# Optimization experiments

Measured on AMD Instinct MI355X. Metric: run time of the kernel, lower is better.

Reference implementation:

```python
import jax, jax.numpy as jnp
import numpy as np


def setup_inputs() -> dict:
    key = jax.random.key(0)
    k1, k2 = jax.random.split(key)
    B, D, L = 32, 64, 4096
    N_CB, K = 4, 512
    x_in = jax.random.normal(k1, (B, D, L), dtype=jnp.float32)
    # torch.rand(num_tokens, token_dim) per codebook -> uniform [0,1)
    codebooks = jax.random.uniform(k2, (N_CB, K, D), dtype=jnp.float32)
    return {"x_in": x_in, "codebooks": codebooks}


def _vq_select(x_res, emb):
    """Nearest-code quantization for one codebook.

    x_res: [B, D, L], emb: [K, D]
    Returns z_q [B, D, L], idx [B, L].
    """
    x_t = jnp.transpose(x_res, (0, 2, 1))  # [B, L, D]
    # squared euclidean distances via GEMM (same argmin as torch.cdist)
    d2 = (
        jnp.sum(x_t * x_t, axis=-1, keepdims=True)
        - 2.0 * jnp.einsum("bld,kd->blk", x_t, emb)
        + jnp.sum(emb * emb, axis=-1)
    )  # [B, L, K]
    idx = jnp.argmin(d2, axis=-1)  # [B, L]
    z_q = jnp.transpose(emb[idx], (0, 2, 1))  # [B, D, L]
    return z_q, idx


def reference(x_in, codebooks):
    """Residual VQ: per codebook quantize the residual, accumulate sums.

    Returns z_q_aggregated [B, n_cb, D, L] (cumulative sums) and
    indices [B, L, n_cb].
    """
    n_cb = codebooks.shape[0]
    x_res = x_in
    z_q = jnp.zeros_like(x_in)
    agg = []
    idx_list = []
    for c in range(n_cb):  # small fixed loop over codebooks
        z_q_ind, idx = _vq_select(x_res, codebooks[c])
        x_res = x_res - z_q_ind
        z_q = z_q + z_q_ind
        agg.append(z_q)
        idx_list.append(idx)
    z_q_aggregated = jnp.stack(agg, axis=1)  # [B, n_cb, D, L]
    indices = jnp.stack(idx_list, axis=-1)  # [B, L, n_cb]
    return z_q_aggregated, indices
```

## Files before the change

kernel.cpp:

```cpp
#include <hip/hip_runtime.h>


#define LL   4096
#define DD   64
#define KK   512
#define NCB  4
#define TB   32
#define NTHR 256
#define XS   36
#define ES   260
#define EBUFN (16 * ES)

#define ZQ_ELEMS (32LL * NCB * DD * LL)

__device__ __forceinline__ float np_pairwise_sq64(const float* p) {
#pragma clang fp contract(off)
    float r[8];
#pragma unroll
    for (int j = 0; j < 8; ++j) { float s = p[j] * p[j]; r[j] = s; }
#pragma unroll
    for (int i = 8; i < 64; i += 8)
#pragma unroll
        for (int j = 0; j < 8; ++j) { float s = p[i + j] * p[i + j]; r[j] = r[j] + s; }
    return ((r[0] + r[1]) + (r[2] + r[3])) + ((r[4] + r[5]) + (r[6] + r[7]));
}

__global__ void se_kernel(const float* __restrict__ cb, float* __restrict__ se) {
    int t = blockIdx.x * blockDim.x + threadIdx.x;
    if (t >= NCB * KK) return;
    se[t] = np_pairwise_sq64(cb + (size_t)t * DD);
}

__global__ __launch_bounds__(NTHR) void rvq_kernel(const float* __restrict__ x_in,
                                                   const float* __restrict__ cb,
                                                   const float* __restrict__ se,
                                                   float* __restrict__ out) {
    __shared__ float ebuf[EBUFN];
    __shared__ float x_lds[DD * XS];

    const int tid  = threadIdx.x;
    const int lane = tid & 63;
    const int w8   = (tid >> 6) << 3;

    const long T0 = (long)blockIdx.x * TB;
    const int b  = (int)(T0 >> 12);
    const int l0 = (int)(T0 & 4095);

    {
        const float* xb = x_in + (size_t)b * DD * LL + l0;
        const int dd0 = tid >> 3;
        const int t4  = (tid & 7) << 2;
#pragma unroll
        for (int it = 0; it < 2; ++it) {
            const int d = it * 32 + dd0;
            const float4 v = *reinterpret_cast<const float4*>(xb + (size_t)d * LL + t4);
            *reinterpret_cast<float4*>(&x_lds[d * XS + t4]) = v;
        }
    }

    const int sq = tid & 3;
    const int sk = tid >> 2;

    float4 sv0, sv1, sv2, sv3;
    {
        const float* ec = cb + (size_t)(sq << 2);
        sv0 = *reinterpret_cast<const float4*>(ec + (size_t)(sk +   0) * DD);
        sv1 = *reinterpret_cast<const float4*>(ec + (size_t)(sk +  64) * DD);
        sv2 = *reinterpret_cast<const float4*>(ec + (size_t)(sk + 128) * DD);
        sv3 = *reinterpret_cast<const float4*>(ec + (size_t)(sk + 192) * DD);
    }

    __syncthreads();

    float zq[8];
#pragma unroll
    for (int t = 0; t < 8; ++t) zq[t] = 0.f;

    const int sxj = lane & 7;
    const int sxt = lane >> 3;
    const int myt = lane & 7;
    const int da  = lane >> 3;

#pragma unroll 1
    for (int c = 0; c < NCB; ++c) {
        float a3;
        {
            float r;
            {
#pragma clang fp contract(off)
                float p = x_lds[sxj * XS + w8 + sxt];
                r = p * p;
#pragma unroll
                for (int i = 1; i < 8; ++i) {
                    float q = x_lds[(i * 8 + sxj) * XS + w8 + sxt];
                    r = r + q * q;
                }
            }
            float o1 = __shfl_xor(r, 1, 64);
            float a1 = r + o1;
            float o2 = __shfl_xor(a1, 2, 64);
            float a2 = a1 + o2;
            float o4 = __shfl_xor(a2, 4, 64);
            a3 = a2 + o4;
        }

        float b1v[8]; int b1i[8];
#pragma unroll
        for (int t = 0; t < 8; ++t) { b1v[t] = __builtin_inff(); b1i[t] = 0; }

        float acc[8][4];

#pragma unroll 1
        for (int s = 0; s < 8; ++s) {
            ebuf[(sq * 4 + 0) * ES + sk      ] = sv0.x;
            ebuf[(sq * 4 + 1) * ES + sk      ] = sv0.y;
            ebuf[(sq * 4 + 2) * ES + sk      ] = sv0.z;
            ebuf[(sq * 4 + 3) * ES + sk      ] = sv0.w;
            ebuf[(sq * 4 + 0) * ES + sk +  64] = sv1.x;
            ebuf[(sq * 4 + 1) * ES + sk +  64] = sv1.y;
            ebuf[(sq * 4 + 2) * ES + sk +  64] = sv1.z;
            ebuf[(sq * 4 + 3) * ES + sk +  64] = sv1.w;
            ebuf[(sq * 4 + 0) * ES + sk + 128] = sv2.x;
            ebuf[(sq * 4 + 1) * ES + sk + 128] = sv2.y;
            ebuf[(sq * 4 + 2) * ES + sk + 128] = sv2.z;
            ebuf[(sq * 4 + 3) * ES + sk + 128] = sv2.w;
            ebuf[(sq * 4 + 0) * ES + sk + 192] = sv3.x;
            ebuf[(sq * 4 + 1) * ES + sk + 192] = sv3.y;
            ebuf[(sq * 4 + 2) * ES + sk + 192] = sv3.z;
            ebuf[(sq * 4 + 3) * ES + sk + 192] = sv3.w;

            __syncthreads();

            {
                int nc = c, ns = s + 1;
                if (ns == 8) { nc = c + 1; ns = 0; }
                if (nc < NCB) {
                    const float* ec = cb + ((size_t)(nc * KK + (ns >> 2) * 256)) * DD
                                         + (size_t)((ns & 3) * 16 + (sq << 2));
                    sv0 = *reinterpret_cast<const float4*>(ec + (size_t)(sk +   0) * DD);
                    sv1 = *reinterpret_cast<const float4*>(ec + (size_t)(sk +  64) * DD);
                    sv2 = *reinterpret_cast<const float4*>(ec + (size_t)(sk + 128) * DD);
                    sv3 = *reinterpret_cast<const float4*>(ec + (size_t)(sk + 192) * DD);
                }
            }

            if ((s & 3) == 0) {
#pragma unroll
                for (int t = 0; t < 8; ++t)
#pragma unroll
                    for (int g = 0; g < 4; ++g) acc[t][g] = 0.f;
            }

            const int mbase = (s & 3) * 16;
#pragma unroll
            for (int dd = 0; dd < 16; ++dd) {
                const int d = mbase + dd;
                const float4 e4  = *reinterpret_cast<const float4*>(&ebuf[dd * ES + (lane << 2)]);
                const float4 xa  = *reinterpret_cast<const float4*>(&x_lds[d * XS + w8]);
                const float4 xb4 = *reinterpret_cast<const float4*>(&x_lds[d * XS + w8 + 4]);
#define FMA4(T, XV)                                   \
                acc[T][0] = fmaf(XV, e4.x, acc[T][0]); \
                acc[T][1] = fmaf(XV, e4.y, acc[T][1]); \
                acc[T][2] = fmaf(XV, e4.z, acc[T][2]); \
                acc[T][3] = fmaf(XV, e4.w, acc[T][3]);
                FMA4(0, xa.x)  FMA4(1, xa.y)  FMA4(2, xa.z)  FMA4(3, xa.w)
                FMA4(4, xb4.x) FMA4(5, xb4.y) FMA4(6, xb4.z) FMA4(7, xb4.w)
#undef FMA4
            }

            if ((s & 3) == 3) {
#pragma clang fp contract(off)
                const int kb = (s >> 2) * 256 + (lane << 2);
                const float4 se4 = *reinterpret_cast<const float4*>(&se[c * KK + kb]);
                const float sev[4] = {se4.x, se4.y, se4.z, se4.w};
#pragma unroll
                for (int t = 0; t < 8; ++t) {
                    const float sxv = __shfl(a3, t << 3, 64);
#pragma unroll
                    for (int g = 0; g < 4; ++g) {
                        const float twod = 2.0f * acc[t][g];
                        const float d2 = (sxv - twod) + sev[g];
                        if (d2 < b1v[t]) { b1v[t] = d2; b1i[t] = kb + g; }
                    }
                }
            }

            __syncthreads();
        }

#pragma unroll
        for (int t = 0; t < 8; ++t) {
            float v = b1v[t]; int i = b1i[t];
#pragma unroll
            for (int off = 32; off > 0; off >>= 1) {
                const float ov = __shfl_xor(v, off, 64);
                const int   oi = __shfl_xor(i, off, 64);
                if (ov < v || (ov == v && oi < i)) { v = ov; i = oi; }
            }
            b1i[t] = i;
        }

        int kown = 0;
#pragma unroll
        for (int t = 0; t < 8; ++t) if (myt == t) kown = b1i[t];

        {
#pragma clang fp contract(off)
            const float* erow = cb + ((size_t)(c * KK) + kown) * DD + da;
#pragma unroll
            for (int i = 0; i < 8; ++i) {
                const float ev = erow[i * 8];
                const int xi = (i * 8 + da) * XS + w8 + myt;
                x_lds[xi] = x_lds[xi] - ev;
                zq[i] = zq[i] + ev;
            }
        }

#pragma unroll
        for (int t = 0; t < 8; ++t)
            if (lane == t)
                out[ZQ_ELEMS + ((size_t)b * LL + l0 + w8 + t) * NCB + c] = (float)b1i[t];

#pragma unroll
        for (int i = 0; i < 8; ++i)
            ebuf[(i * 8 + da) * XS + w8 + myt] = zq[i];
        __syncthreads();
        {
            float* zo = out + (((size_t)b * NCB + c) * DD) * LL + l0;
            const int c4 = (tid & 7) << 2;
            const int d0 = tid >> 3;
#pragma unroll
            for (int p = 0; p < 2; ++p) {
                const int d = p * 32 + d0;
                const float4 v = *reinterpret_cast<const float4*>(&ebuf[d * XS + c4]);
                *reinterpret_cast<float4*>(zo + (size_t)d * LL + c4) = v;
            }
        }
        __syncthreads();
    }
}

extern "C" void kernel_launch(void* const* d_in, const int* in_sizes, int n_in,
                              void* d_out, int out_size, void* d_ws, size_t ws_size,
                              hipStream_t stream) {
    const float* x_in = (const float*)d_in[0];
    const float* cb   = (const float*)d_in[1];
    float* out = (float*)d_out;
    float* se  = (float*)d_ws;

    se_kernel<<<dim3((NCB * KK + 255) / 256), dim3(256), 0, stream>>>(cb, se);
    rvq_kernel<<<dim3((32 * LL) / TB), dim3(NTHR), 0, stream>>>(x_in, cb, se, out);
}
```

Baseline: 639.0 us.

## Double block tile to 64 tokens with 512 threads sharing each codebook slice

Each block now handles 64 tokens with 512 threads instead of 32 with 256, so each codebook slice staged in shared memory is reused by twice as many tokens and global codebook traffic per token halves. Staging loads per thread shrink to two float4s. The z_q output transpose is done in two halves through the smaller shared buffer, which adds barriers. The first accumulation step multiplies instead of zeroing then adding. Larger blocks give fewer resident blocks per CU and half as many blocks overall.

```diff
diff --git a/kernel.cpp b/kernel.cpp
--- a/kernel.cpp
+++ b/kernel.cpp
@@ -5,9 +5,9 @@
 #define DD   64
 #define KK   512
 #define NCB  4
-#define TB   32
-#define NTHR 256
-#define XS   36
+#define TB   64
+#define NTHR 512
+#define XS   68
 #define ES   260
 #define EBUFN (16 * ES)
 
@@ -35,7 +35,7 @@
                                                    const float* __restrict__ cb,
                                                    const float* __restrict__ se,
                                                    float* __restrict__ out) {
-    __shared__ float ebuf[EBUFN];
+    __shared__ float sbuf[EBUFN];
     __shared__ float x_lds[DD * XS];
 
     const int tid  = threadIdx.x;
@@ -48,27 +48,24 @@
 
     {
         const float* xb = x_in + (size_t)b * DD * LL + l0;
-        const int dd0 = tid >> 3;
-        const int t4  = (tid & 7) << 2;
 #pragma unroll
         for (int it = 0; it < 2; ++it) {
-            const int d = it * 32 + dd0;
-            const float4 v = *reinterpret_cast<const float4*>(xb + (size_t)d * LL + t4);
-            *reinterpret_cast<float4*>(&x_lds[d * XS + t4]) = v;
+            const int q = tid + it * NTHR;
+            const int d = q >> 4;
+            const int col = (q & 15) << 2;
+            const float4 v = *reinterpret_cast<const float4*>(xb + (size_t)d * LL + col);
+            *reinterpret_cast<float4*>(&x_lds[d * XS + col]) = v;
         }
     }
 
     const int sq = tid & 3;
     const int sk = tid >> 2;
-
-    float4 sv0, sv1, sv2, sv3;
-    {
-        const float* ec = cb + (size_t)(sq << 2);
-        sv0 = *reinterpret_cast<const float4*>(ec + (size_t)(sk +   0) * DD);
-        sv1 = *reinterpret_cast<const float4*>(ec + (size_t)(sk +  64) * DD);
-        sv2 = *reinterpret_cast<const float4*>(ec + (size_t)(sk + 128) * DD);
-        sv3 = *reinterpret_cast<const float4*>(ec + (size_t)(sk + 192) * DD);
-    }
+    const size_t toff = (size_t)sk * DD + (sq << 2);
+    const int r0 = (sq << 2) * ES + sk;
+
+    float4 sv0, sv1;
+    sv0 = *reinterpret_cast<const float4*>(cb + toff);
+    sv1 = *reinterpret_cast<const float4*>(cb + toff + (size_t)128 * DD);
 
     __syncthreads();
 
@@ -96,12 +93,9 @@
                     r = r + q * q;
                 }
             }
-            float o1 = __shfl_xor(r, 1, 64);
-            float a1 = r + o1;
-            float o2 = __shfl_xor(a1, 2, 64);
-            float a2 = a1 + o2;
-            float o4 = __shfl_xor(a2, 4, 64);
-            a3 = a2 + o4;
+            float o1 = __shfl_xor(r, 1, 64);  float a1 = r + o1;
+            float o2 = __shfl_xor(a1, 2, 64); float a2 = a1 + o2;
+            float o4 = __shfl_xor(a2, 4, 64); a3 = a2 + o4;
         }
 
         float b1v[8]; int b1i[8];
@@ -112,22 +106,14 @@
 
 #pragma unroll 1
         for (int s = 0; s < 8; ++s) {
-            ebuf[(sq * 4 + 0) * ES + sk      ] = sv0.x;
-            ebuf[(sq * 4 + 1) * ES + sk      ] = sv0.y;
-            ebuf[(sq * 4 + 2) * ES + sk      ] = sv0.z;
-            ebuf[(sq * 4 + 3) * ES + sk      ] = sv0.w;
-            ebuf[(sq * 4 + 0) * ES + sk +  64] = sv1.x;
-            ebuf[(sq * 4 + 1) * ES + sk +  64] = sv1.y;
-            ebuf[(sq * 4 + 2) * ES + sk +  64] = sv1.z;
-            ebuf[(sq * 4 + 3) * ES + sk +  64] = sv1.w;
-            ebuf[(sq * 4 + 0) * ES + sk + 128] = sv2.x;
-            ebuf[(sq * 4 + 1) * ES + sk + 128] = sv2.y;
-            ebuf[(sq * 4 + 2) * ES + sk + 128] = sv2.z;
-            ebuf[(sq * 4 + 3) * ES + sk + 128] = sv2.w;
-            ebuf[(sq * 4 + 0) * ES + sk + 192] = sv3.x;
-            ebuf[(sq * 4 + 1) * ES + sk + 192] = sv3.y;
-            ebuf[(sq * 4 + 2) * ES + sk + 192] = sv3.z;
-            ebuf[(sq * 4 + 3) * ES + sk + 192] = sv3.w;
+            sbuf[r0         ]        = sv0.x;
+            sbuf[r0 +     ES]        = sv0.y;
+            sbuf[r0 + 2 * ES]        = sv0.z;
+            sbuf[r0 + 3 * ES]        = sv0.w;
+            sbuf[r0          + 128]  = sv1.x;
+            sbuf[r0 +     ES + 128]  = sv1.y;
+            sbuf[r0 + 2 * ES + 128]  = sv1.z;
+            sbuf[r0 + 3 * ES + 128]  = sv1.w;
 
             __syncthreads();
 
@@ -136,37 +122,53 @@
                 if (ns == 8) { nc = c + 1; ns = 0; }
                 if (nc < NCB) {
                     const float* ec = cb + ((size_t)(nc * KK + (ns >> 2) * 256)) * DD
-                                         + (size_t)((ns & 3) * 16 + (sq << 2));
-                    sv0 = *reinterpret_cast<const float4*>(ec + (size_t)(sk +   0) * DD);
-                    sv1 = *reinterpret_cast<const float4*>(ec + (size_t)(sk +  64) * DD);
-                    sv2 = *reinterpret_cast<const float4*>(ec + (size_t)(sk + 128) * DD);
-                    sv3 = *reinterpret_cast<const float4*>(ec + (size_t)(sk + 192) * DD);
-                }
-            }
+                                         + ((ns & 3) << 4);
+                    sv0 = *reinterpret_cast<const float4*>(ec + toff);
+                    sv1 = *reinterpret_cast<const float4*>(ec + toff + (size_t)128 * DD);
+                }
+            }
+
+            const int mbase = (s & 3) * 16;
+
+#define EX_LOADS(D)                                                                           \
+            const float4 e4 = *reinterpret_cast<const float4*>(&sbuf[(D - mbase) * ES + (lane << 2)]); \
+            const float4 xa = *reinterpret_cast<const float4*>(&x_lds[(D) * XS + w8]);        \
+            const float4 xb4 = *reinterpret_cast<const float4*>(&x_lds[(D) * XS + w8 + 4]);
+#define FMA4(T, XV)                                   \
+            acc[T][0] = fmaf(XV, e4.x, acc[T][0]);    \
+            acc[T][1] = fmaf(XV, e4.y, acc[T][1]);    \
+            acc[T][2] = fmaf(XV, e4.z, acc[T][2]);    \
+            acc[T][3] = fmaf(XV, e4.w, acc[T][3]);
+#define MUL4(T, XV)                                   \
+            acc[T][0] = XV * e4.x;                    \
+            acc[T][1] = XV * e4.y;                    \
+            acc[T][2] = XV * e4.z;                    \
+            acc[T][3] = XV * e4.w;
 
             if ((s & 3) == 0) {
-#pragma unroll
-                for (int t = 0; t < 8; ++t)
-#pragma unroll
-                    for (int g = 0; g < 4; ++g) acc[t][g] = 0.f;
-            }
-
-            const int mbase = (s & 3) * 16;
-#pragma unroll
-            for (int dd = 0; dd < 16; ++dd) {
-                const int d = mbase + dd;
-                const float4 e4  = *reinterpret_cast<const float4*>(&ebuf[dd * ES + (lane << 2)]);
-                const float4 xa  = *reinterpret_cast<const float4*>(&x_lds[d * XS + w8]);
-                const float4 xb4 = *reinterpret_cast<const float4*>(&x_lds[d * XS + w8 + 4]);
-#define FMA4(T, XV)                                   \
-                acc[T][0] = fmaf(XV, e4.x, acc[T][0]); \
-                acc[T][1] = fmaf(XV, e4.y, acc[T][1]); \
-                acc[T][2] = fmaf(XV, e4.z, acc[T][2]); \
-                acc[T][3] = fmaf(XV, e4.w, acc[T][3]);
-                FMA4(0, xa.x)  FMA4(1, xa.y)  FMA4(2, xa.z)  FMA4(3, xa.w)
-                FMA4(4, xb4.x) FMA4(5, xb4.y) FMA4(6, xb4.z) FMA4(7, xb4.w)
+                {
+                    EX_LOADS(0)
+                    MUL4(0, xa.x) MUL4(1, xa.y) MUL4(2, xa.z) MUL4(3, xa.w)
+                    MUL4(4, xb4.x) MUL4(5, xb4.y) MUL4(6, xb4.z) MUL4(7, xb4.w)
+                }
+#pragma unroll
+                for (int dd = 1; dd < 16; ++dd) {
+                    EX_LOADS(dd)
+                    FMA4(0, xa.x) FMA4(1, xa.y) FMA4(2, xa.z) FMA4(3, xa.w)
+                    FMA4(4, xb4.x) FMA4(5, xb4.y) FMA4(6, xb4.z) FMA4(7, xb4.w)
+                }
+            } else {
+#pragma unroll
+                for (int dd = 0; dd < 16; ++dd) {
+                    const int d = mbase + dd;
+                    EX_LOADS(d)
+                    FMA4(0, xa.x) FMA4(1, xa.y) FMA4(2, xa.z) FMA4(3, xa.w)
+                    FMA4(4, xb4.x) FMA4(5, xb4.y) FMA4(6, xb4.z) FMA4(7, xb4.w)
+                }
+            }
+#undef MUL4
 #undef FMA4
-            }
+#undef EX_LOADS
 
             if ((s & 3) == 3) {
 #pragma clang fp contract(off)
@@ -221,22 +223,25 @@
             if (lane == t)
                 out[ZQ_ELEMS + ((size_t)b * LL + l0 + w8 + t) * NCB + c] = (float)b1i[t];
 
-#pragma unroll
-        for (int i = 0; i < 8; ++i)
-            ebuf[(i * 8 + da) * XS + w8 + myt] = zq[i];
-        __syncthreads();
         {
             float* zo = out + (((size_t)b * NCB + c) * DD) * LL + l0;
-            const int c4 = (tid & 7) << 2;
-            const int d0 = tid >> 3;
 #pragma unroll
             for (int p = 0; p < 2; ++p) {
-                const int d = p * 32 + d0;
-                const float4 v = *reinterpret_cast<const float4*>(&ebuf[d * XS + c4]);
-                *reinterpret_cast<float4*>(zo + (size_t)d * LL + c4) = v;
-            }
-        }
-        __syncthreads();
+#pragma unroll
+                for (int i = 0; i < 4; ++i) {
+                    const int ii = p * 4 + i;
+                    sbuf[(ii * 8 + da - 32 * p) * XS + w8 + myt] = zq[ii];
+                }
+                __syncthreads();
+                {
+                    const int dloc = tid >> 4;
+                    const int col  = (tid & 15) << 2;
+                    const float4 v = *reinterpret_cast<const float4*>(&sbuf[dloc * XS + col]);
+                    *reinterpret_cast<float4*>(zo + (size_t)(32 * p + dloc) * LL + col) = v;
+                }
+                __syncthreads();
+            }
+        }
     }
 }
 
```

Measured after the change: 667.0 us. 4.4% more time.
